# Kernel optimization log

Hardware: AMD Instinct MI355X
Metric: run time of the kernel (lower is better)

Reference implementation:

```python
import jax, jax.numpy as jnp
import numpy as np

B, D_IN, D_HID, D_OUT = 32768, 512, 1024, 2048

def setup_inputs() -> dict:
    key = jax.random.key(0)
    k1, k2, k3, k4 = jax.random.split(key, 4)
    x = jax.random.normal(k1, (B, D_IN), dtype=jnp.float32)
    # linear1 params (torch Linear default-style init, scale approximated)
    l1_w = jax.random.normal(k2, (D_HID, D_IN), dtype=jnp.float32) * (D_IN ** -0.5)
    l1_b = jax.random.normal(k3, (D_HID,), dtype=jnp.float32) * 0.01
    # second linear params: normal(0, hidden^-0.5) weight, zero bias as in source
    weight = jax.random.normal(k4, (D_OUT, D_HID), dtype=jnp.float32) * (D_HID ** -0.5)
    bias = jnp.zeros((D_OUT,), dtype=jnp.float32)
    return {"x": x, "l1_w": l1_w, "l1_b": l1_b, "weight": weight, "bias": bias}

def reference(x, l1_w, l1_b, weight, bias):
    # linear1: [B, D_IN] -> [B, D_HID]
    h = jnp.einsum('bi,hi->bh', x, l1_w) + l1_b
    # fused linear + max epilogue: scores [B, D_OUT] -> max over output dim
    scores = jnp.einsum('bh,oh->bo', h, weight) + bias
    return jnp.max(scores, axis=-1)  # [B]
```

## Files before the change

kernel.cpp:

```cpp
#include <hip/hip_runtime.h>
#include <hip/hip_bf16.h>
#include <stdint.h>

static constexpr int BATCH = 32768;
static constexpr int DIN   = 512;
static constexpr int DHID  = 1024;
static constexpr int DOUT  = 2048;

typedef __bf16 bf16x8 __attribute__((ext_vector_type(8)));
typedef float  f32x4  __attribute__((ext_vector_type(4)));

__device__ __forceinline__ unsigned short f2bf(float f) {
    unsigned int u = __float_as_uint(f);
    u += 0x7FFFu + ((u >> 16) & 1u);
    return (unsigned short)(u >> 16);
}

__device__ __forceinline__ void gload_lds16(const void* g, void* l) {
    __builtin_amdgcn_global_load_lds((__attribute__((address_space(1))) void*)g,
                                     (__attribute__((address_space(3))) void*)l,
                                     16, 0, 0);
}


__global__ __launch_bounds__(256) void prep_kernel(
    const float* __restrict__ w1, const float4* __restrict__ w2f,
    const float4* __restrict__ xf, const float* __restrict__ b1,
    const float* __restrict__ b2,
    unsigned short* __restrict__ w1t, ushort4* __restrict__ w2b,
    ushort4* __restrict__ xb, float* __restrict__ bp) {
    const int blk = blockIdx.x;
    const int t   = threadIdx.x;
    if (blk < 512) {
        __shared__ float tile[32][33];
        const int tileI = blk & 15;
        const int tileH = blk >> 4;
        const int iBase = tileI * 32, hBase = tileH * 32;
        const int col = t & 31, rowq = t >> 5;
#pragma unroll
        for (int p = 0; p < 4; ++p) {
            const int row = p * 8 + rowq;
            tile[row][col] = w1[(size_t)(hBase + row) * DIN + iBase + col];
        }
        __syncthreads();
#pragma unroll
        for (int p = 0; p < 4; ++p) {
            const int row = p * 8 + rowq;
            w1t[(size_t)(iBase + row) * DHID + hBase + col] = f2bf(tile[col][row]);
        }
    } else if (blk < 2560) {
        __shared__ float wsum[4];
        const int o = blk - 512;
        const size_t g = (size_t)o * 256 + t;
        float4 v = w2f[g];
        ushort4 ob;
        ob.x = f2bf(v.x); ob.y = f2bf(v.y); ob.z = f2bf(v.z); ob.w = f2bf(v.w);
        w2b[g] = ob;
        float4 bv = ((const float4*)b1)[t];
        float s = v.x * bv.x + v.y * bv.y + v.z * bv.z + v.w * bv.w;
#pragma unroll
        for (int off = 1; off < 64; off <<= 1) s += __shfl_xor(s, off);
        if ((t & 63) == 0) wsum[t >> 6] = s;
        __syncthreads();
        if (t == 0) bp[o] = wsum[0] + wsum[1] + wsum[2] + wsum[3] + b2[o];
    } else {
        const size_t g = (size_t)(blk - 2560) * 256 + t;
        float4 v = xf[g];
        ushort4 o;
        o.x = f2bf(v.x); o.y = f2bf(v.y); o.z = f2bf(v.z); o.w = f2bf(v.w);
        xb[g] = o;
    }
}

__global__ __launch_bounds__(256) void gemmW_kernel(
    const unsigned short* __restrict__ A,
    const unsigned short* __restrict__ Bw,
    unsigned short* __restrict__ W) {
    constexpr int K = DHID;
    __shared__ __align__(16) unsigned short sA[64 * 128];
    __shared__ __align__(16) unsigned short sB[64 * 128];

    const int tid  = threadIdx.x;
    const int lane = tid & 63;
    const int wid  = tid >> 6;
    const int wr = wid >> 1, wc = wid & 1;
    const int r = lane & 15, q = lane >> 4;
    const int blockN = blockIdx.x * 64;
    const int blockM = blockIdx.y * 64;

    const int chKey = (tid & 15) ^ ((tid >> 4) & 15);
    const size_t aBase = (size_t)(blockM + (tid >> 4)) * K + chKey * 8;
    const size_t bBase = (size_t)(blockN + (tid >> 4)) * K + chKey * 8;

    f32x4 acc[2][2];
#pragma unroll
    for (int mt = 0; mt < 2; ++mt)
#pragma unroll
        for (int nt = 0; nt < 2; ++nt) { f32x4 z = {0.f, 0.f, 0.f, 0.f}; acc[mt][nt] = z; }

    for (int k0 = 0; k0 < K; k0 += 128) {
#pragma unroll
        for (int j = 0; j < 4; ++j) {
            gload_lds16(A  + aBase + (size_t)j * 16 * K + k0, sA + j * 2048 + wid * 512);
            gload_lds16(Bw + bBase + (size_t)j * 16 * K + k0, sB + j * 2048 + wid * 512);
        }
        __syncthreads();
#pragma unroll
        for (int ks = 0; ks < 4; ++ks) {
            const int ch = ((ks << 2) + q) ^ r;
            bf16x8 af[2], bf[2];
#pragma unroll
            for (int mt = 0; mt < 2; ++mt) af[mt] = *(const bf16x8*)&sA[(wr * 32 + mt * 16 + r) * 128 + ch * 8];
#pragma unroll
            for (int nt = 0; nt < 2; ++nt) bf[nt] = *(const bf16x8*)&sB[(wc * 32 + nt * 16 + r) * 128 + ch * 8];
#pragma unroll
            for (int mt = 0; mt < 2; ++mt)
#pragma unroll
                for (int nt = 0; nt < 2; ++nt)
                    acc[mt][nt] = __builtin_amdgcn_mfma_f32_16x16x32_bf16(af[mt], bf[nt], acc[mt][nt], 0, 0, 0);
        }
        __syncthreads();
    }

#pragma unroll
    for (int mt = 0; mt < 2; ++mt) {
        const int row0 = blockM + wr * 32 + mt * 16 + q * 4;
#pragma unroll
        for (int nt = 0; nt < 2; ++nt) {
            const int col = blockN + wc * 32 + nt * 16 + r;
#pragma unroll
            for (int reg = 0; reg < 4; ++reg)
                W[(size_t)(row0 + reg) * DIN + col] = f2bf(acc[mt][nt][reg]);
        }
    }
}

__global__ __launch_bounds__(256) void gemmS_kernel(
    const unsigned short* __restrict__ A,
    const unsigned short* __restrict__ Bw,
    const float* __restrict__ bp,
    float* __restrict__ partials) {
    constexpr int K = DIN;
    __shared__ __align__(16) unsigned short sA[128 * 64];
    __shared__ __align__(16) unsigned short sB[128 * 64];

    const int tid  = threadIdx.x;
    const int lane = tid & 63;
    const int wid  = tid >> 6;
    const int wr = wid >> 1, wc = wid & 1;
    const int r = lane & 15, q = lane >> 4;
    const int sw = r & 7;

    const int g    = blockIdx.x;
    const int xcd  = g & 7;
    const int i    = g >> 3;
    const int nIdx = i & 15;
    const int blockM = (xcd * 32 + (i >> 4)) * 128;
    const int blockN = nIdx * 128;

    const int chKey = (lane & 7) ^ (lane >> 3);
    const size_t aBase = (size_t)(blockM + wid * 32 + (lane >> 3)) * K + chKey * 8;
    const size_t bBase = (size_t)(blockN + wid * 32 + (lane >> 3)) * K + chKey * 8;

    f32x4 acc[4][4];
#pragma unroll
    for (int mt = 0; mt < 4; ++mt)
#pragma unroll
        for (int nt = 0; nt < 4; ++nt) { f32x4 z = {0.f, 0.f, 0.f, 0.f}; acc[mt][nt] = z; }

    for (int k0 = 0; k0 < K; k0 += 64) {
#pragma unroll
        for (int j = 0; j < 4; ++j) {
            gload_lds16(A  + aBase + (size_t)j * 8 * K + k0, sA + wid * 2048 + j * 512);
            gload_lds16(Bw + bBase + (size_t)j * 8 * K + k0, sB + wid * 2048 + j * 512);
        }
        __syncthreads();
#pragma unroll
        for (int ks = 0; ks < 2; ++ks) {
            const int ch = ((ks << 2) + q) ^ sw;
            bf16x8 af[4], bf[4];
#pragma unroll
            for (int mt = 0; mt < 4; ++mt) af[mt] = *(const bf16x8*)&sA[(wr * 64 + mt * 16 + r) * 64 + ch * 8];
#pragma unroll
            for (int nt = 0; nt < 4; ++nt) bf[nt] = *(const bf16x8*)&sB[(wc * 64 + nt * 16 + r) * 64 + ch * 8];
#pragma unroll
            for (int mt = 0; mt < 4; ++mt)
#pragma unroll
                for (int nt = 0; nt < 4; ++nt)
                    acc[mt][nt] = __builtin_amdgcn_mfma_f32_16x16x32_bf16(af[mt], bf[nt], acc[mt][nt], 0, 0, 0);
        }
        __syncthreads();
    }

    const int colBase = blockN + wc * 64;
    const int rowBase = blockM + wr * 64;
    float bv[4];
#pragma unroll
    for (int nt = 0; nt < 4; ++nt) bv[nt] = bp[colBase + nt * 16 + r];

    float mx[4][4];
#pragma unroll
    for (int mt = 0; mt < 4; ++mt)
#pragma unroll
        for (int reg = 0; reg < 4; ++reg) {
            float v = acc[mt][0][reg] + bv[0];
            v = fmaxf(v, acc[mt][1][reg] + bv[1]);
            v = fmaxf(v, acc[mt][2][reg] + bv[2]);
            v = fmaxf(v, acc[mt][3][reg] + bv[3]);
            mx[mt][reg] = v;
        }
#pragma unroll
    for (int off = 1; off < 16; off <<= 1)
#pragma unroll
        for (int mt = 0; mt < 4; ++mt)
#pragma unroll
            for (int reg = 0; reg < 4; ++reg)
                mx[mt][reg] = fmaxf(mx[mt][reg], __shfl_xor(mx[mt][reg], off));

    if (r == 0) {
#pragma unroll
        for (int mt = 0; mt < 4; ++mt)
#pragma unroll
            for (int reg = 0; reg < 4; ++reg) {
                const int row = rowBase + mt * 16 + q * 4 + reg;
                partials[(size_t)row * 32 + nIdx * 2 + wc] = mx[mt][reg];
            }
    }
}

__global__ __launch_bounds__(256) void reduce_kernel(
    const float4* __restrict__ partials, float* __restrict__ out) {
    const int row = blockIdx.x * blockDim.x + threadIdx.x;
    const float4* p = partials + (size_t)row * 8;
    float m = -INFINITY;
#pragma unroll
    for (int i = 0; i < 8; ++i) {
        float4 v = p[i];
        m = fmaxf(m, fmaxf(fmaxf(v.x, v.y), fmaxf(v.z, v.w)));
    }
    out[row] = m;
}

extern "C" void kernel_launch(void* const* d_in, const int* in_sizes, int n_in,
                              void* d_out, int out_size, void* d_ws, size_t ws_size,
                              hipStream_t stream) {
    const float* x   = (const float*)d_in[0];
    const float* l1w = (const float*)d_in[1];
    const float* l1b = (const float*)d_in[2];
    const float* w2  = (const float*)d_in[3];
    const float* b2  = (const float*)d_in[4];
    float* out = (float*)d_out;

    char* ws = (char*)d_ws;
    unsigned short* w1t = (unsigned short*)(ws);
    unsigned short* w2b = (unsigned short*)(ws + 1048576);
    unsigned short* Wb  = (unsigned short*)(ws + 5242880);
    float* bp           = (float*)(ws + 7340032);
    unsigned short* xb  = (unsigned short*)(ws + 7348224);
    float* partials     = (float*)(ws + 40902656);

    prep_kernel<<<18944, 256, 0, stream>>>(
        l1w, (const float4*)w2, (const float4*)x, l1b, b2,
        w1t, (ushort4*)w2b, (ushort4*)xb, bp);

    gemmW_kernel<<<dim3(DIN / 64, DOUT / 64), 256, 0, stream>>>(w2b, w1t, Wb);

    gemmS_kernel<<<4096, 256, 0, stream>>>(xb, Wb, bp, partials);

    reduce_kernel<<<BATCH / 256, 256, 0, stream>>>((const float4*)partials, out);
}
```

Baseline: 204.3 us.

## Rewrite main GEMM as 256x256-tile, 8-wave double-buffered pipelined kernel

The main x·W' GEMM moves from 128x128 tiles with 4 waves and a synchronous load-then-compute loop to 256x256 tiles with 8 waves. LDS is double-buffered and async global-to-LDS loads are interleaved with MFMA phases using explicit vmcnt/lgkmcnt waits, barriers and setprio. The aim is to hide global load latency behind matrix math and to raise data reuse per loaded tile. The costs are a 128KB LDS footprint, 128 accumulator registers per thread, and a hand-scheduled loop hardcoded to K=512 that is fragile if any sizes change.

```diff
diff --git a/kernel.cpp b/kernel.cpp
--- a/kernel.cpp
+++ b/kernel.cpp
@@ -135,96 +135,154 @@
     }
 }
 
-__global__ __launch_bounds__(256) void gemmS_kernel(
+__global__ __launch_bounds__(512, 2) void gemmS_kernel(
     const unsigned short* __restrict__ A,
     const unsigned short* __restrict__ Bw,
     const float* __restrict__ bp,
     float* __restrict__ partials) {
     constexpr int K = DIN;
-    __shared__ __align__(16) unsigned short sA[128 * 64];
-    __shared__ __align__(16) unsigned short sB[128 * 64];
+    __shared__ __align__(16) unsigned short lds[65536];
 
     const int tid  = threadIdx.x;
     const int lane = tid & 63;
     const int wid  = tid >> 6;
-    const int wr = wid >> 1, wc = wid & 1;
-    const int r = lane & 15, q = lane >> 4;
-    const int sw = r & 7;
+    const int wr   = wid >> 2;
+    const int wc   = wid & 3;
+    const int r    = lane & 15, q = lane >> 4;
 
     const int g    = blockIdx.x;
     const int xcd  = g & 7;
     const int i    = g >> 3;
-    const int nIdx = i & 15;
-    const int blockM = (xcd * 32 + (i >> 4)) * 128;
-    const int blockN = nIdx * 128;
-
-    const int chKey = (lane & 7) ^ (lane >> 3);
-    const size_t aBase = (size_t)(blockM + wid * 32 + (lane >> 3)) * K + chKey * 8;
-    const size_t bBase = (size_t)(blockN + wid * 32 + (lane >> 3)) * K + chKey * 8;
-
-    f32x4 acc[4][4];
-#pragma unroll
-    for (int mt = 0; mt < 4; ++mt)
+    const int mIdx = xcd * 16 + (i >> 3);
+    const int nIdx = i & 7;
+    const int blockM = mIdx * 256;
+    const int blockN = nIdx * 256;
+
+    const int sRow = tid >> 2;
+    const int swz  = (tid & 3) ^ ((tid >> 3) & 3);
+    const unsigned short* aSrc = A  + (size_t)(blockM + sRow) * K + swz * 8;
+    const unsigned short* bSrc = Bw + (size_t)(blockN + sRow) * K + swz * 8;
+    unsigned short* ldsW = lds + wid * 512;
+
+#define STAGE(srcPtr, isB, buf, kh, kt) do {                                    \
+    gload_lds16((srcPtr) + (kt) * 64 + (kh) * 32,                               \
+                ldsW + (buf) * 32768 + (isB) * 16384 + (kh) * 8192);            \
+    gload_lds16((srcPtr) + 128 * K + (kt) * 64 + (kh) * 32,                     \
+                ldsW + (buf) * 32768 + (isB) * 16384 + (kh) * 8192 + 4096);     \
+} while (0)
+
+    const int rsw  = (r >> 1) & 3;
+    const int fOff = (q ^ rsw) * 8;
+    const unsigned short* ldsAf = lds + (wr * 128 + r) * 32 + fOff;
+    const unsigned short* ldsBf = lds + 16384 + (wc * 64 + r) * 32 + fOff;
+
+    f32x4 acc[8][4];
+#pragma unroll
+    for (int mt = 0; mt < 8; ++mt)
 #pragma unroll
         for (int nt = 0; nt < 4; ++nt) { f32x4 z = {0.f, 0.f, 0.f, 0.f}; acc[mt][nt] = z; }
-
-    for (int k0 = 0; k0 < K; k0 += 64) {
-#pragma unroll
-        for (int j = 0; j < 4; ++j) {
-            gload_lds16(A  + aBase + (size_t)j * 8 * K + k0, sA + wid * 2048 + j * 512);
-            gload_lds16(Bw + bBase + (size_t)j * 8 * K + k0, sB + wid * 2048 + j * 512);
-        }
-        __syncthreads();
-#pragma unroll
-        for (int ks = 0; ks < 2; ++ks) {
-            const int ch = ((ks << 2) + q) ^ sw;
-            bf16x8 af[4], bf[4];
-#pragma unroll
-            for (int mt = 0; mt < 4; ++mt) af[mt] = *(const bf16x8*)&sA[(wr * 64 + mt * 16 + r) * 64 + ch * 8];
-#pragma unroll
-            for (int nt = 0; nt < 4; ++nt) bf[nt] = *(const bf16x8*)&sB[(wc * 64 + nt * 16 + r) * 64 + ch * 8];
-#pragma unroll
-            for (int mt = 0; mt < 4; ++mt)
-#pragma unroll
-                for (int nt = 0; nt < 4; ++nt)
-                    acc[mt][nt] = __builtin_amdgcn_mfma_f32_16x16x32_bf16(af[mt], bf[nt], acc[mt][nt], 0, 0, 0);
-        }
-        __syncthreads();
-    }
+    bf16x8 af[4], bfr[4];
+
+#define LDA(buf, ks, mg) do {                                                   \
+    const unsigned short* p_ = ldsAf + (buf) * 32768 + (ks) * 8192 + (mg) * 2048; \
+    af[0] = *(const bf16x8*)(p_);                                               \
+    af[1] = *(const bf16x8*)(p_ + 512);                                         \
+    af[2] = *(const bf16x8*)(p_ + 1024);                                        \
+    af[3] = *(const bf16x8*)(p_ + 1536);                                        \
+} while (0)
+#define LDB(buf, ks) do {                                                       \
+    const unsigned short* p_ = ldsBf + (buf) * 32768 + (ks) * 8192;             \
+    bfr[0] = *(const bf16x8*)(p_);                                              \
+    bfr[1] = *(const bf16x8*)(p_ + 512);                                        \
+    bfr[2] = *(const bf16x8*)(p_ + 1024);                                       \
+    bfr[3] = *(const bf16x8*)(p_ + 1536);                                       \
+} while (0)
+#define MM(mg) do {                                                             \
+    __builtin_amdgcn_s_setprio(1);                                              \
+    _Pragma("unroll") for (int m_ = 0; m_ < 4; ++m_)                            \
+    _Pragma("unroll") for (int n_ = 0; n_ < 4; ++n_)                            \
+        acc[(mg) * 4 + m_][n_] = __builtin_amdgcn_mfma_f32_16x16x32_bf16(       \
+            af[m_], bfr[n_], acc[(mg) * 4 + m_][n_], 0, 0, 0);                  \
+    __builtin_amdgcn_s_setprio(0);                                              \
+} while (0)
+#define BAR()   __builtin_amdgcn_s_barrier()
+#define LGKM0() asm volatile("s_waitcnt lgkmcnt(0)" ::: "memory")
+#define VMC(n)  asm volatile("s_waitcnt vmcnt(" #n ")" ::: "memory")
+
+    STAGE(bSrc, 1, 0, 0, 0);
+    STAGE(aSrc, 0, 0, 0, 0);
+    STAGE(bSrc, 1, 0, 1, 0);
+    STAGE(aSrc, 0, 0, 1, 0);
+    STAGE(bSrc, 1, 1, 0, 1);
+    STAGE(aSrc, 0, 1, 0, 1);
+    STAGE(bSrc, 1, 1, 1, 1);
+    VMC(6);
+    BAR();
+
+#pragma unroll 1
+    for (int it = 0; it < 3; ++it) {
+        const int t1 = 2 * it + 1, n0 = 2 * it + 2, n1 = 2 * it + 3;
+        LDA(0, 0, 0); LDB(0, 0); STAGE(aSrc, 0, 1, 1, t1);
+        BAR(); LGKM0(); MM(0); BAR();
+        LDA(0, 0, 1); STAGE(bSrc, 1, 0, 0, n0);
+        BAR(); LGKM0(); MM(1); BAR();
+        LDA(0, 1, 0); LDB(0, 1); STAGE(aSrc, 0, 0, 0, n0);
+        BAR(); LGKM0(); MM(0); BAR();
+        LDA(0, 1, 1); STAGE(bSrc, 1, 0, 1, n0); VMC(6);
+        BAR(); LGKM0(); MM(1); BAR();
+        LDA(1, 0, 0); LDB(1, 0); STAGE(aSrc, 0, 0, 1, n0);
+        BAR(); LGKM0(); MM(0); BAR();
+        LDA(1, 0, 1); STAGE(bSrc, 1, 1, 0, n1);
+        BAR(); LGKM0(); MM(1); BAR();
+        LDA(1, 1, 0); LDB(1, 1); STAGE(aSrc, 0, 1, 0, n1);
+        BAR(); LGKM0(); MM(0); BAR();
+        LDA(1, 1, 1); STAGE(bSrc, 1, 1, 1, n1); VMC(6);
+        BAR(); LGKM0(); MM(1); BAR();
+    }
+    LDA(0, 0, 0); LDB(0, 0); STAGE(aSrc, 0, 1, 1, 7);
+    BAR(); LGKM0(); MM(0); BAR();
+    LDA(0, 0, 1);
+    BAR(); LGKM0(); MM(1); BAR();
+    LDA(0, 1, 0); LDB(0, 1);
+    BAR(); LGKM0(); MM(0); BAR();
+    LDA(0, 1, 1); VMC(0);
+    BAR(); LGKM0(); MM(1); BAR();
+    LDA(1, 0, 0); LDB(1, 0);
+    BAR(); LGKM0(); MM(0); BAR();
+    LDA(1, 0, 1);
+    BAR(); LGKM0(); MM(1); BAR();
+    LDA(1, 1, 0); LDB(1, 1);
+    BAR(); LGKM0(); MM(0); BAR();
+    LDA(1, 1, 1);
+    BAR(); LGKM0(); MM(1);
+
+#undef STAGE
+#undef LDA
+#undef LDB
+#undef MM
+#undef BAR
+#undef LGKM0
+#undef VMC
 
     const int colBase = blockN + wc * 64;
-    const int rowBase = blockM + wr * 64;
     float bv[4];
 #pragma unroll
     for (int nt = 0; nt < 4; ++nt) bv[nt] = bp[colBase + nt * 16 + r];
 
-    float mx[4][4];
-#pragma unroll
-    for (int mt = 0; mt < 4; ++mt)
+#pragma unroll
+    for (int mt = 0; mt < 8; ++mt) {
 #pragma unroll
         for (int reg = 0; reg < 4; ++reg) {
-            float v = acc[mt][0][reg] + bv[0];
-            v = fmaxf(v, acc[mt][1][reg] + bv[1]);
-            v = fmaxf(v, acc[mt][2][reg] + bv[2]);
-            v = fmaxf(v, acc[mt][3][reg] + bv[3]);
-            mx[mt][reg] = v;
-        }
-#pragma unroll
-    for (int off = 1; off < 16; off <<= 1)
-#pragma unroll
-        for (int mt = 0; mt < 4; ++mt)
-#pragma unroll
-            for (int reg = 0; reg < 4; ++reg)
-                mx[mt][reg] = fmaxf(mx[mt][reg], __shfl_xor(mx[mt][reg], off));
-
-    if (r == 0) {
-#pragma unroll
-        for (int mt = 0; mt < 4; ++mt)
-#pragma unroll
-            for (int reg = 0; reg < 4; ++reg) {
-                const int row = rowBase + mt * 16 + q * 4 + reg;
-                partials[(size_t)row * 32 + nIdx * 2 + wc] = mx[mt][reg];
+            float v = fmaxf(fmaxf(acc[mt][0][reg] + bv[0], acc[mt][1][reg] + bv[1]),
+                            fmaxf(acc[mt][2][reg] + bv[2], acc[mt][3][reg] + bv[3]));
+#pragma unroll
+            for (int off = 1; off < 16; off <<= 1)
+                v = fmaxf(v, __shfl_xor(v, off));
+            if (r == 0) {
+                const int row = blockM + wr * 128 + mt * 16 + q * 4 + reg;
+                partials[(size_t)row * 32 + nIdx * 4 + wc] = v;
             }
+        }
     }
 }
 
@@ -265,7 +323,7 @@
 
     gemmW_kernel<<<dim3(DIN / 64, DOUT / 64), 256, 0, stream>>>(w2b, w1t, Wb);
 
-    gemmS_kernel<<<4096, 256, 0, stream>>>(xb, Wb, bp, partials);
+    gemmS_kernel<<<1024, 512, 0, stream>>>(xb, Wb, bp, partials);
 
     reduce_kernel<<<BATCH / 256, 256, 0, stream>>>((const float4*)partials, out);
 }
```

Result: faster. 192.7 us (-5.7%).
